# Optimization experiments

Measured on AMD Instinct MI355X. Metric: run time of the kernel, lower is better.

Reference implementation:

```python
import jax, jax.numpy as jnp
import numpy as np
from itertools import combinations

SEQ_LEN = 8
FEAT = 2048
SET_SIZE = 2
DOUT = 1152
WAY = 5
SHOT = 5
NQ = 500
MAX_LEN = int(SEQ_LEN * 1.5)
LN_EPS = 1e-5

TUPLES = np.array(list(combinations(range(SEQ_LEN), SET_SIZE)), dtype=np.int32)  # [T, SET_SIZE]
T_LEN = TUPLES.shape[0]  # C(8,2) = 28

def _positional_encoding(d_model, max_len):
    pos = np.arange(max_len, dtype=np.float32)[:, None]
    div = np.exp(np.arange(0, d_model, 2, dtype=np.float32) * (-np.log(10000.0) / d_model))
    pe = np.zeros((max_len, d_model), dtype=np.float32)
    pe[:, 0::2] = np.sin(pos * div)
    pe[:, 1::2] = np.cos(pos * div)
    return jnp.asarray(pe)

PE = _positional_encoding(FEAT, MAX_LEN)  # dropout is identity in eval mode

def _layernorm(x, gamma, beta):
    mu = jnp.mean(x, axis=-1, keepdims=True)
    var = jnp.var(x, axis=-1, keepdims=True)
    return (x - mu) * jax.lax.rsqrt(var + LN_EPS) * gamma + beta

def setup_inputs() -> dict:
    key = jax.random.key(0)
    ks = jax.random.split(key, 8)
    din = FEAT * SET_SIZE
    sc = 1.0 / np.sqrt(din)
    return {
        "support_set": jax.random.normal(ks[0], (WAY * SHOT, SEQ_LEN, FEAT), jnp.float32),
        "support_labels": jnp.repeat(jnp.arange(WAY, dtype=jnp.int32), SHOT),  # sorted, balanced episode
        "queries": jax.random.normal(ks[1], (NQ, SEQ_LEN, FEAT), jnp.float32),
        "k_w": jax.random.normal(ks[2], (din, DOUT), jnp.float32) * sc,
        "k_b": jnp.zeros((DOUT,), jnp.float32),
        "v_w": jax.random.normal(ks[3], (din, DOUT), jnp.float32) * sc,
        "v_b": jnp.zeros((DOUT,), jnp.float32),
        "ln_k_gamma": jnp.ones((DOUT,), jnp.float32),
        "ln_k_beta": jnp.zeros((DOUT,), jnp.float32),
        "global_temperature": jnp.asarray(1.0, jnp.float32),
        "temperature_weight": jnp.ones((1,), jnp.float32),
    }

def reference(support_set, support_labels, queries, k_w, k_b, v_w, v_b,
              ln_k_gamma, ln_k_beta, global_temperature, temperature_weight):
    n_q = queries.shape[0]
    # positional encoding (dropout is eval-mode identity)
    s = support_set + PE[:SEQ_LEN]
    q = queries + PE[:SEQ_LEN]
    # gather frame tuples: [n, T, SET_SIZE, FEAT] -> [n, T, SET_SIZE*FEAT]
    s_t = s[:, TUPLES, :].reshape(WAY * SHOT, T_LEN, SET_SIZE * FEAT)
    q_t = q[:, TUPLES, :].reshape(n_q, T_LEN, SET_SIZE * FEAT)
    # K / V projections; LayerNorm only on K (as in the module)
    s_ks = _layernorm(s_t @ k_w + k_b, ln_k_gamma, ln_k_beta)
    q_ks = _layernorm(q_t @ k_w + k_b, ln_k_gamma, ln_k_beta)
    s_vs = s_t @ v_w + v_b
    q_vs = q_t @ v_w + v_b
    # labels are sorted & balanced -> per-class slices are a reshape
    class_k = s_ks.reshape(WAY, SHOT, T_LEN, DOUT)
    class_v = s_vs.reshape(WAY, SHOT, T_LEN, DOUT)
    # scores[c,q,t,k,u] = <q_ks[q,t], class_k[c,k,u]> / sqrt(DOUT)
    scores = jnp.einsum('qtd,ckud->cqtku', q_ks, class_k) / np.sqrt(DOUT)
    # softmax jointly over (support-clip k, support-tuple u) per query tuple t
    attn = jax.nn.softmax(scores.reshape(WAY, n_q, T_LEN, SHOT * T_LEN), axis=-1)
    attn = attn.reshape(WAY, n_q, T_LEN, SHOT, T_LEN)
    # prototype = sum over support clips of attn @ class_v
    proto = jnp.einsum('cqtku,ckud->cqtd', attn, class_v)  # [WAY, NQ, T, DOUT]
    diff = q_vs[None] - proto
    dist = jnp.sum(diff * diff, axis=(-2, -1)) / T_LEN  # [WAY, NQ]
    logits = (-dist * global_temperature * temperature_weight[0]).T  # [NQ, WAY]
    return logits
```

## Files before the change

kernel.cpp:

```cpp
#include <hip/hip_runtime.h>

typedef __bf16 bf16;
typedef __attribute__((ext_vector_type(8))) __bf16 bf16x8;
typedef __attribute__((ext_vector_type(4))) float f32x4;

#define AS1 __attribute__((address_space(1)))
#define AS3 __attribute__((address_space(3)))

__device__ __constant__ int c_T0[28] = {0,0,0,0,0,0,0,1,1,1,1,1,1,2,2,2,2,2,3,3,3,3,4,4,4,5,5,6};
__device__ __constant__ int c_T1[28] = {1,2,3,4,5,6,7,2,3,4,5,6,7,3,4,5,6,7,4,5,6,7,5,6,7,6,7,7};

__global__ __launch_bounds__(256) void fill_pack(
    const float* __restrict__ queries, const float* __restrict__ support,
    const float* __restrict__ kw, const float* __restrict__ vw,
    bf16* __restrict__ X, bf16* __restrict__ Wp)
{
    __shared__ float t[32][33];
    const int tid = threadIdx.x;
    if (blockIdx.x < 4224) {
        const int f = blockIdx.x;
        bf16* row = X + (long)f * 2048;
        const int d0 = tid << 3;
        if (f >= 4200) {
            bf16x8 z;
            #pragma unroll
            for (int i = 0; i < 8; ++i) z[i] = (bf16)0.f;
            *(bf16x8*)(row + d0) = z;
            return;
        }
        const float* src = (f < 4000) ? (queries + (long)f * 2048)
                                      : (support + (long)(f - 4000) * 2048);
        const int s = f & 7;
        bf16x8 o;
        #pragma unroll
        for (int i = 0; i < 8; ++i) {
            int d = d0 + i;
            float dv = __expf((float)(d >> 1) * -0.008994473019508f);
            float ang = (float)s * dv;
            float pe = (d & 1) ? __cosf(ang) : __sinf(ang);
            o[i] = (bf16)(src[d] + pe);
        }
        *(bf16x8*)(row + d0) = o;
    } else {
        const int b = blockIdx.x - 4224;
        const int k0 = (b & 63) << 5, n0g = (b >> 6) << 5;
        const int tx = tid & 31, ty = tid >> 5;
        const int j = n0g / 1152, nc = n0g % 1152;
        const float* src = ((j < 2) ? kw : vw) + (long)(((j & 1) << 11) + k0) * 1152 + nc;
        #pragma unroll
        for (int i = 0; i < 4; ++i)
            t[ty + (i << 3)][tx] = src[(long)(ty + (i << 3)) * 1152 + tx];
        __syncthreads();
        #pragma unroll
        for (int i = 0; i < 4; ++i)
            Wp[(long)(n0g + ty + (i << 3)) * 2048 + k0 + tx] = (bf16)t[tx][ty + (i << 3)];
    }
}

template <typename OutT>
__global__ __launch_bounds__(256) void gemm_bt(
    const bf16* __restrict__ A, long lda, const bf16* __restrict__ B, long ldb,
    OutT* __restrict__ C, int N, int K, float scale, int tiles_n)
{
    __shared__ __align__(16) bf16 lA[128 * 32];
    __shared__ __align__(16) bf16 lB[128 * 32];
    const int tid = threadIdx.x;
    const int wid = tid >> 6, lane = tid & 63;
    const int wm = (wid >> 1) << 6, wn = (wid & 1) << 6;
    const int quad = lane >> 4, l16 = lane & 15;
    const int tm = blockIdx.x / tiles_n, tn = blockIdx.x % tiles_n;
    const int m0 = tm << 7, n0 = tn << 7;
    const bf16* Abase = A + (long)m0 * lda;

    f32x4 acc[4][4];
    #pragma unroll
    for (int i = 0; i < 4; ++i)
        #pragma unroll
        for (int j = 0; j < 4; ++j)
            #pragma unroll
            for (int r = 0; r < 4; ++r) acc[i][j][r] = 0.f;

    const int srow = lane >> 2, scol = (lane & 3) << 3;
    for (int kk = 0; kk < K; kk += 32) {
        __syncthreads();
        #pragma unroll
        for (int p = 0; p < 2; ++p) {
            const int rbase = (wid << 5) + (p << 4);
            const bf16* ga = Abase + (long)(rbase + srow) * lda + kk + scol;
            const bf16* gb = B + (long)(n0 + rbase + srow) * ldb + kk + scol;
            __builtin_amdgcn_global_load_lds((const AS1 unsigned int*)ga,
                                             (AS3 unsigned int*)(lA + rbase * 32), 16, 0, 0);
            __builtin_amdgcn_global_load_lds((const AS1 unsigned int*)gb,
                                             (AS3 unsigned int*)(lB + rbase * 32), 16, 0, 0);
        }
        __builtin_amdgcn_s_waitcnt(0);
        __syncthreads();
        bf16x8 af[4], bfr[4];
        #pragma unroll
        for (int i = 0; i < 4; ++i)
            af[i] = *(const bf16x8*)(lA + (wm + (i << 4) + l16) * 32 + (quad << 3));
        #pragma unroll
        for (int j = 0; j < 4; ++j)
            bfr[j] = *(const bf16x8*)(lB + (wn + (j << 4) + l16) * 32 + (quad << 3));
        #pragma unroll
        for (int i = 0; i < 4; ++i)
            #pragma unroll
            for (int j = 0; j < 4; ++j)
                acc[i][j] = __builtin_amdgcn_mfma_f32_16x16x32_bf16(af[i], bfr[j], acc[i][j], 0, 0, 0);
    }
    #pragma unroll
    for (int i = 0; i < 4; ++i) {
        const int row = m0 + wm + (i << 4) + (quad << 2);
        #pragma unroll
        for (int j = 0; j < 4; ++j) {
            const int col = n0 + wn + (j << 4) + l16;
            OutT* cp = C + (long)row * N + col;
            #pragma unroll
            for (int r = 0; r < 4; ++r) cp[(long)r * N] = (OutT)(acc[i][j][r] * scale);
        }
    }
}

__global__ __launch_bounds__(256) void gemm_frames(
    const bf16* __restrict__ H, const bf16* __restrict__ Bk,
    const bf16* __restrict__ svs, float* __restrict__ FG, bf16* __restrict__ Gb)
{
    __shared__ __align__(16) bf16 lA[128 * 32];
    __shared__ __align__(16) bf16 lB[128 * 32];
    const int tid = threadIdx.x;
    const int wid = tid >> 6, lane = tid & 63;
    const int wm = (wid >> 1) << 6, wn = (wid & 1) << 6;
    const int quad = lane >> 4, l16 = lane & 15;
    const bool gram = (int)blockIdx.x >= 792;
    int seg = 4, tm, tn;
    const bf16* Abase;
    long la;
    const bf16* B;
    if (!gram) {
        seg = blockIdx.x / 198;
        int r = blockIdx.x % 198;
        tm = r / 6; tn = r % 6;
        Abase = H + seg * 1152 + (long)(tm << 7) * 4608;
        la = 4608;
        B = (seg < 2) ? Bk : svs;
    } else {
        int r = blockIdx.x - 792;
        tm = r / 6; tn = r % 6;
        Abase = svs + (long)(tm << 7) * 1152;
        la = 1152;
        B = svs;
    }
    const int n0 = tn << 7;

    f32x4 acc[4][4];
    #pragma unroll
    for (int i = 0; i < 4; ++i)
        #pragma unroll
        for (int j = 0; j < 4; ++j)
            #pragma unroll
            for (int r = 0; r < 4; ++r) acc[i][j][r] = 0.f;

    const int srow = lane >> 2, scol = (lane & 3) << 3;
    for (int kk = 0; kk < 1152; kk += 32) {
        __syncthreads();
        #pragma unroll
        for (int p = 0; p < 2; ++p) {
            const int rbase = (wid << 5) + (p << 4);
            const bf16* ga = Abase + (long)(rbase + srow) * la + kk + scol;
            const bf16* gb = B + (long)(n0 + rbase + srow) * 1152 + kk + scol;
            __builtin_amdgcn_global_load_lds((const AS1 unsigned int*)ga,
                                             (AS3 unsigned int*)(lA + rbase * 32), 16, 0, 0);
            __builtin_amdgcn_global_load_lds((const AS1 unsigned int*)gb,
                                             (AS3 unsigned int*)(lB + rbase * 32), 16, 0, 0);
        }
        __builtin_amdgcn_s_waitcnt(0);
        __syncthreads();
        bf16x8 af[4], bfr[4];
        #pragma unroll
        for (int i = 0; i < 4; ++i)
            af[i] = *(const bf16x8*)(lA + (wm + (i << 4) + l16) * 32 + (quad << 3));
        #pragma unroll
        for (int j = 0; j < 4; ++j)
            bfr[j] = *(const bf16x8*)(lB + (wn + (j << 4) + l16) * 32 + (quad << 3));
        #pragma unroll
        for (int i = 0; i < 4; ++i)
            #pragma unroll
            for (int j = 0; j < 4; ++j)
                acc[i][j] = __builtin_amdgcn_mfma_f32_16x16x32_bf16(af[i], bfr[j], acc[i][j], 0, 0, 0);
    }
    #pragma unroll
    for (int i = 0; i < 4; ++i) {
        const int rloc = (tm << 7) + wm + (i << 4) + (quad << 2);
        #pragma unroll
        for (int j = 0; j < 4; ++j) {
            const int col = n0 + wn + (j << 4) + l16;
            #pragma unroll
            for (int r = 0; r < 4; ++r) {
                const int row = rloc + r;
                if (!gram) {
                    FG[(long)(seg * 4224 + row) * 768 + col] = acc[i][j][r];
                } else {
                    bool keep = (row < 700) && (col < 700) && (row / 140 == col / 140);
                    Gb[(long)row * 768 + col] = keep ? (bf16)acc[i][j][r] : (bf16)0.f;
                }
            }
        }
    }
}

__global__ __launch_bounds__(256) void proj_support(
    const bf16* __restrict__ H, const float* __restrict__ kb,
    const float* __restrict__ vb, const float* __restrict__ gamma,
    const float* __restrict__ beta,
    bf16* __restrict__ Bk, bf16* __restrict__ svs,
    float* __restrict__ gd, float* __restrict__ kbd,
    float* __restrict__ bd2, float* __restrict__ bdot)
{
    const int u = blockIdx.x, tid = threadIdx.x;
    bf16* outK = Bk + (long)u * 1152;
    bf16* outV = svs + (long)u * 1152;
    if (u >= 700) {
        for (int d = tid; d < 1152; d += 256) { outK[d] = (bf16)0.f; outV[d] = (bf16)0.f; }
        if (tid == 0) { gd[u] = 0.f; kbd[u] = 0.f; bd2[u] = 0.f; bdot[u] = 0.f; }
        return;
    }
    const int n = u / 28, t = u - n * 28;
    const int fi = 4000 + (n << 3) + c_T0[t];
    const int fj = 4000 + (n << 3) + c_T1[t];
    const bf16* Hi = H + (long)fi * 4608;
    const bf16* Hj = H + (long)fj * 4608;
    float xv[5];
    float sum = 0.f, sumsq = 0.f;
    #pragma unroll
    for (int it = 0; it < 5; ++it) {
        int d = tid + (it << 8);
        float x = 0.f;
        if (d < 1152) {
            x = (float)Hi[d] + (float)Hj[1152 + d] + kb[d];
            sum += x; sumsq += x * x;
        }
        xv[it] = x;
    }
    #pragma unroll
    for (int off = 32; off > 0; off >>= 1) {
        sum += __shfl_xor(sum, off, 64);
        sumsq += __shfl_xor(sumsq, off, 64);
    }
    __shared__ float s1[4], s2[4], sr[4][4];
    const int wid = tid >> 6;
    if ((tid & 63) == 0) { s1[wid] = sum; s2[wid] = sumsq; }
    __syncthreads();
    sum = s1[0] + s1[1] + s1[2] + s1[3];
    sumsq = s2[0] + s2[1] + s2[2] + s2[3];
    const float mu = sum * (1.f / 1152.f);
    const float var = sumsq * (1.f / 1152.f) - mu * mu;
    const float rs = rsqrtf(var + 1e-5f);
    float g_ = 0.f, k_ = 0.f, b_ = 0.f, v_ = 0.f;
    #pragma unroll
    for (int it = 0; it < 5; ++it) {
        int d = tid + (it << 8);
        if (d < 1152) {
            float gm = gamma[d];
            float sk = (xv[it] - mu) * rs * gm + beta[d];
            outK[d] = (bf16)(gm * sk);
            g_ += gm * sk;
            k_ += kb[d] * gm * sk;
            b_ += beta[d] * sk;
            float sv = (float)Hi[2304 + d] + (float)Hj[3456 + d] + vb[d];
            outV[d] = (bf16)sv;
            v_ += vb[d] * sv;
        }
    }
    #pragma unroll
    for (int off = 32; off > 0; off >>= 1) {
        g_ += __shfl_xor(g_, off, 64);
        k_ += __shfl_xor(k_, off, 64);
        b_ += __shfl_xor(b_, off, 64);
        v_ += __shfl_xor(v_, off, 64);
    }
    if ((tid & 63) == 0) { sr[wid][0] = g_; sr[wid][1] = k_; sr[wid][2] = b_; sr[wid][3] = v_; }
    __syncthreads();
    if (tid == 0) {
        gd[u]   = sr[0][0] + sr[1][0] + sr[2][0] + sr[3][0];
        kbd[u]  = sr[0][1] + sr[1][1] + sr[2][1] + sr[3][1];
        bd2[u]  = sr[0][2] + sr[1][2] + sr[2][2] + sr[3][2];
        bdot[u] = sr[0][3] + sr[1][3] + sr[2][3] + sr[3][3];
    }
}

__global__ __launch_bounds__(256) void row_stats(
    const bf16* __restrict__ H, const float* __restrict__ kb,
    const float* __restrict__ vb, float* __restrict__ MU,
    float* __restrict__ RS, float* __restrict__ QS)
{
    const bool kside = (int)blockIdx.x < 500;
    const int q = kside ? blockIdx.x : blockIdx.x - 500;
    const int co = kside ? 0 : 2304;
    const float* bias = kside ? kb : vb;
    const int tid = threadIdx.x;
    __shared__ __align__(16) bf16 Ft[8 * 1152];
    __shared__ __align__(16) bf16 Fb[8 * 1152];
    __shared__ float Sa[8], Qa[8], Ca[8], Sb_[8], Qb_[8], Cb_[8], Pp[28], Sk2[2];
    for (int idx = tid; idx < 1152; idx += 256) {
        int row = idx / 144, col = (idx - row * 144) << 3;
        const bf16* src = H + (long)((q << 3) + row) * 4608 + co;
        *(bf16x8*)(Ft + row * 1152 + col) = *(const bf16x8*)(src + col);
        *(bf16x8*)(Fb + row * 1152 + col) = *(const bf16x8*)(src + 1152 + col);
    }
    __syncthreads();
    const int wid = tid >> 6, lane = tid & 63;
    for (int task = wid; task < 45; task += 4) {
        float s0 = 0.f, s1 = 0.f, s2 = 0.f;
        if (task < 16) {
            const bf16* p = (task < 8) ? (Ft + task * 1152) : (Fb + (task - 8) * 1152);
            for (int c = lane << 3; c < 1152; c += 512) {
                bf16x8 v = *(const bf16x8*)(p + c);
                #pragma unroll
                for (int k = 0; k < 8; ++k) {
                    float f = (float)v[k];
                    s0 += f; s1 += f * f; s2 += f * bias[c + k];
                }
            }
        } else if (task < 44) {
            int t = task - 16;
            const bf16* pa = Ft + c_T0[t] * 1152;
            const bf16* pb = Fb + c_T1[t] * 1152;
            for (int c = lane << 3; c < 1152; c += 512) {
                bf16x8 a = *(const bf16x8*)(pa + c);
                bf16x8 b = *(const bf16x8*)(pb + c);
                #pragma unroll
                for (int k = 0; k < 8; ++k) s0 += (float)a[k] * (float)b[k];
            }
        } else {
            for (int c = lane << 3; c < 1152; c += 512) {
                #pragma unroll
                for (int k = 0; k < 8; ++k) { float f = bias[c + k]; s0 += f; s1 += f * f; }
            }
        }
        #pragma unroll
        for (int off = 32; off > 0; off >>= 1) {
            s0 += __shfl_xor(s0, off, 64);
            s1 += __shfl_xor(s1, off, 64);
            s2 += __shfl_xor(s2, off, 64);
        }
        if (lane == 0) {
            if (task < 8)       { Sa[task] = s0; Qa[task] = s1; Ca[task] = s2; }
            else if (task < 16) { Sb_[task - 8] = s0; Qb_[task - 8] = s1; Cb_[task - 8] = s2; }
            else if (task < 44) Pp[task - 16] = s0;
            else                { Sk2[0] = s0; Sk2[1] = s1; }
        }
    }
    __syncthreads();
    if (kside) {
        if (tid < 28) {
            int i = c_T0[tid], j = c_T1[tid];
            float mu = (Sa[i] + Sb_[j] + Sk2[0]) * (1.f / 1152.f);
            float ex2 = (Qa[i] + Qb_[j] + Sk2[1] + 2.f * (Pp[tid] + Ca[i] + Cb_[j])) * (1.f / 1152.f);
            float var = ex2 - mu * mu;
            int m = q * 28 + tid;
            MU[m] = mu;
            RS[m] = rsqrtf(var + 1e-5f);
        }
    } else {
        if (tid < 64) {
            float term = 0.f;
            if (lane < 28) {
                int i = c_T0[lane], j = c_T1[lane];
                term = Qa[i] + Qb_[j] + Sk2[1] + 2.f * (Pp[lane] + Ca[i] + Cb_[j]);
            }
            #pragma unroll
            for (int off = 32; off > 0; off >>= 1) term += __shfl_xor(term, off, 64);
            if (lane == 0) QS[q] = term;
        }
    }
}

__global__ __launch_bounds__(320) void assemble_softmax(
    const float* __restrict__ Fkt, const float* __restrict__ Fkb,
    const float* __restrict__ MU, const float* __restrict__ RS,
    const float* __restrict__ gd, const float* __restrict__ kbd,
    const float* __restrict__ bd2, bf16* __restrict__ attn)
{
    const int m = blockIdx.x, tid = threadIdx.x;
    bf16* arow = attn + (long)m * 768;
    if (m >= 14000) {
        for (int d = tid; d < 768; d += 320) arow[d] = (bf16)0.f;
        return;
    }
    if (tid < 68) arow[700 + tid] = (bf16)0.f;
    const int q = m / 28, t = m - q * 28;
    const float* ft = Fkt + (long)((q << 3) + c_T0[t]) * 768;
    const float* fb = Fkb + (long)((q << 3) + c_T1[t]) * 768;
    const float mu = MU[m], rs = RS[m];
    const int w = tid >> 6, lane = tid & 63;
    const int base = w * 140;
    const float sc = 0.029462782549439484f;
    int u0 = base + lane, u1 = base + 64 + lane, u2 = base + 128 + lane;
    float v0 = (rs * (ft[u0] + fb[u0] + kbd[u0] - mu * gd[u0]) + bd2[u0]) * sc;
    float v1 = (rs * (ft[u1] + fb[u1] + kbd[u1] - mu * gd[u1]) + bd2[u1]) * sc;
    float v2 = (lane < 12)
             ? (rs * (ft[u2] + fb[u2] + kbd[u2] - mu * gd[u2]) + bd2[u2]) * sc
             : -1e30f;
    float mx = fmaxf(fmaxf(v0, v1), v2);
    #pragma unroll
    for (int off = 32; off > 0; off >>= 1) mx = fmaxf(mx, __shfl_xor(mx, off, 64));
    float e0 = __expf(v0 - mx), e1 = __expf(v1 - mx);
    float e2 = (lane < 12) ? __expf(v2 - mx) : 0.f;
    float s = e0 + e1 + e2;
    #pragma unroll
    for (int off = 32; off > 0; off >>= 1) s += __shfl_xor(s, off, 64);
    const float inv = 1.f / s;
    bf16* aw = arow + base;
    aw[lane] = (bf16)(e0 * inv);
    aw[64 + lane] = (bf16)(e1 * inv);
    if (lane < 12) aw[128 + lane] = (bf16)(e2 * inv);
}

__global__ __launch_bounds__(256) void final_dist(
    const bf16* __restrict__ attn, const bf16* __restrict__ attnG,
    const float* __restrict__ FG, const float* __restrict__ bdot,
    float* __restrict__ dist)
{
    const int w = threadIdx.x >> 6, lane = threadIdx.x & 63;
    const int m = blockIdx.x * 4 + w;
    const int q = m / 28, t = m - q * 28;
    const int fi = (q << 3) + c_T0[t], fj = (q << 3) + c_T1[t];
    const bf16* ar = attn + (long)m * 768;
    const bf16* gr = attnG + (long)m * 768;
    const float* ft = FG + (long)(8448 + fi) * 768;
    const float* fb = FG + (long)(12672 + fj) * 768;
    #pragma unroll
    for (int c = 0; c < 5; ++c) {
        const int base = c * 140;
        float s = 0.f;
        {
            int u = base + lane;
            float wv = ft[u] + fb[u] + bdot[u];
            s += (float)ar[u] * ((float)gr[u] - 2.f * wv);
        }
        {
            int u = base + 64 + lane;
            float wv = ft[u] + fb[u] + bdot[u];
            s += (float)ar[u] * ((float)gr[u] - 2.f * wv);
        }
        if (lane < 12) {
            int u = base + 128 + lane;
            float wv = ft[u] + fb[u] + bdot[u];
            s += (float)ar[u] * ((float)gr[u] - 2.f * wv);
        }
        #pragma unroll
        for (int off = 32; off > 0; off >>= 1) s += __shfl_xor(s, off, 64);
        if (lane == 0) atomicAdd(&dist[c * 500 + q], s);
    }
}

__global__ void finalize(const float* __restrict__ dist, const float* __restrict__ QS,
                         const float* __restrict__ gt, const float* __restrict__ tw,
                         float* __restrict__ out)
{
    int i = blockIdx.x * 256 + threadIdx.x;
    if (i < 2500) {
        int q = i / 5, c = i - q * 5;
        out[i] = -(dist[c * 500 + q] + QS[q]) * (gt[0] * tw[0] * (1.f / 28.f));
    }
}

extern "C" void kernel_launch(void* const* d_in, const int* in_sizes, int n_in,
                              void* d_out, int out_size, void* d_ws, size_t ws_size,
                              hipStream_t stream)
{
    const float* support = (const float*)d_in[0];
    const float* queries = (const float*)d_in[2];
    const float* kw      = (const float*)d_in[3];
    const float* kb      = (const float*)d_in[4];
    const float* vw      = (const float*)d_in[5];
    const float* vb      = (const float*)d_in[6];
    const float* gamma   = (const float*)d_in[7];
    const float* beta    = (const float*)d_in[8];
    const float* gt      = (const float*)d_in[9];
    const float* tw      = (const float*)d_in[10];
    float* out = (float*)d_out;

    char* ws = (char*)d_ws;
    size_t off = 0;
    auto alloc = [&](size_t b) { char* p = ws + off; off += (b + 255) & ~(size_t)255; return p; };
    bf16* X      = (bf16*)alloc(4224ull * 2048 * 2);
    bf16* Wp     = (bf16*)alloc(4608ull * 2048 * 2);
    char* uni    = alloc(14080ull * 768 * 4);
    bf16* H      = (bf16*)uni;
    bf16* attn   = (bf16*)uni;
    bf16* attnG  = (bf16*)(uni + 14080ull * 768 * 2);
    float* FG    = (float*)alloc(16896ull * 768 * 4);
    bf16* Bk     = (bf16*)alloc(768ull * 1152 * 2);
    bf16* svs    = (bf16*)alloc(768ull * 1152 * 2);
    bf16* Gb     = (bf16*)alloc(768ull * 768 * 2);
    float* MU    = (float*)alloc(14000ull * 4);
    float* RS    = (float*)alloc(14000ull * 4);
    float* gd    = (float*)alloc(768 * 4);
    float* kbd   = (float*)alloc(768 * 4);
    float* bd2   = (float*)alloc(768 * 4);
    float* bdot  = (float*)alloc(768 * 4);
    float* QS    = (float*)alloc(500 * 4);
    float* dist  = (float*)alloc(5 * 500 * 4);

    hipMemsetAsync(dist, 0, 5 * 500 * 4, stream);
    fill_pack<<<4224 + 9216, 256, 0, stream>>>(queries, support, kw, vw, X, Wp);
    gemm_bt<bf16><<<33 * 36, 256, 0, stream>>>(X, 2048, Wp, 2048, H, 4608, 2048, 1.f, 36);
    proj_support<<<768, 256, 0, stream>>>(H, kb, vb, gamma, beta, Bk, svs, gd, kbd, bd2, bdot);
    row_stats<<<1000, 256, 0, stream>>>(H, kb, vb, MU, RS, QS);
    gemm_frames<<<828, 256, 0, stream>>>(H, Bk, svs, FG, Gb);
    assemble_softmax<<<14080, 320, 0, stream>>>(FG, FG + 4224ull * 768, MU, RS, gd, kbd, bd2, attn);
    gemm_bt<bf16><<<110 * 6, 256, 0, stream>>>(attn, 768, Gb, 768, attnG, 768, 768, 1.f, 6);
    final_dist<<<3500, 256, 0, stream>>>(attn, attnG, FG, bdot, dist);
    finalize<<<10, 256, 0, stream>>>(dist, QS, gt, tw, out);
}
```

Before: 423.5 us.

## Store frame-gram intermediates in bf16 and merge support/row-stat kernels

The FG intermediate buffer (per-frame projections against support keys/values) is now written and read as bf16 instead of fp32, halving its memory traffic in gemm_frames, assemble_softmax and final_dist. Separately, proj_support and row_stats are fused into one launch with a shared-memory union, removing one kernel launch and letting the two independent workloads run together. The bf16 storage adds rounding error to the attention logits and distance terms, and the merged kernel reserves the larger shared-memory footprint for every block.

```diff
diff --git a/kernel.cpp b/kernel.cpp
--- a/kernel.cpp
+++ b/kernel.cpp
@@ -123,7 +123,7 @@
 
 __global__ __launch_bounds__(256) void gemm_frames(
     const bf16* __restrict__ H, const bf16* __restrict__ Bk,
-    const bf16* __restrict__ svs, float* __restrict__ FG, bf16* __restrict__ Gb)
+    const bf16* __restrict__ svs, bf16* __restrict__ FG, bf16* __restrict__ Gb)
 {
     __shared__ __align__(16) bf16 lA[128 * 32];
     __shared__ __align__(16) bf16 lB[128 * 32];
@@ -198,7 +198,7 @@
             for (int r = 0; r < 4; ++r) {
                 const int row = rloc + r;
                 if (!gram) {
-                    FG[(long)(seg * 4224 + row) * 768 + col] = acc[i][j][r];
+                    FG[(long)(seg * 4224 + row) * 768 + col] = (bf16)acc[i][j][r];
                 } else {
                     bool keep = (row < 700) && (col < 700) && (row / 140 == col / 140);
                     Gb[(long)row * 768 + col] = keep ? (bf16)acc[i][j][r] : (bf16)0.f;
@@ -208,99 +208,108 @@
     }
 }
 
-__global__ __launch_bounds__(256) void proj_support(
+__global__ __launch_bounds__(256) void support_stats(
     const bf16* __restrict__ H, const float* __restrict__ kb,
     const float* __restrict__ vb, const float* __restrict__ gamma,
     const float* __restrict__ beta,
     bf16* __restrict__ Bk, bf16* __restrict__ svs,
     float* __restrict__ gd, float* __restrict__ kbd,
-    float* __restrict__ bd2, float* __restrict__ bdot)
-{
-    const int u = blockIdx.x, tid = threadIdx.x;
-    bf16* outK = Bk + (long)u * 1152;
-    bf16* outV = svs + (long)u * 1152;
-    if (u >= 700) {
-        for (int d = tid; d < 1152; d += 256) { outK[d] = (bf16)0.f; outV[d] = (bf16)0.f; }
-        if (tid == 0) { gd[u] = 0.f; kbd[u] = 0.f; bd2[u] = 0.f; bdot[u] = 0.f; }
+    float* __restrict__ bd2, float* __restrict__ bdot,
+    float* __restrict__ MU, float* __restrict__ RS, float* __restrict__ QS)
+{
+    __shared__ __align__(16) char smem[2 * 9216 * 2 + 512];
+    const int tid = threadIdx.x;
+    const int wid = tid >> 6, lane = tid & 63;
+    if ((int)blockIdx.x < 768) {
+        const int u = blockIdx.x;
+        bf16* outK = Bk + (long)u * 1152;
+        bf16* outV = svs + (long)u * 1152;
+        if (u >= 700) {
+            for (int d = tid; d < 1152; d += 256) { outK[d] = (bf16)0.f; outV[d] = (bf16)0.f; }
+            if (tid == 0) { gd[u] = 0.f; kbd[u] = 0.f; bd2[u] = 0.f; bdot[u] = 0.f; }
+            return;
+        }
+        float* s1 = (float*)smem;
+        float* s2 = s1 + 4;
+        float* sr = s2 + 4;
+        const int n = u / 28, t = u - n * 28;
+        const int fi = 4000 + (n << 3) + c_T0[t];
+        const int fj = 4000 + (n << 3) + c_T1[t];
+        const bf16* Hi = H + (long)fi * 4608;
+        const bf16* Hj = H + (long)fj * 4608;
+        float xv[5];
+        float sum = 0.f, sumsq = 0.f;
+        #pragma unroll
+        for (int it = 0; it < 5; ++it) {
+            int d = tid + (it << 8);
+            float x = 0.f;
+            if (d < 1152) {
+                x = (float)Hi[d] + (float)Hj[1152 + d] + kb[d];
+                sum += x; sumsq += x * x;
+            }
+            xv[it] = x;
+        }
+        #pragma unroll
+        for (int off = 32; off > 0; off >>= 1) {
+            sum += __shfl_xor(sum, off, 64);
+            sumsq += __shfl_xor(sumsq, off, 64);
+        }
+        if ((tid & 63) == 0) { s1[wid] = sum; s2[wid] = sumsq; }
+        __syncthreads();
+        sum = s1[0] + s1[1] + s1[2] + s1[3];
+        sumsq = s2[0] + s2[1] + s2[2] + s2[3];
+        const float mu = sum * (1.f / 1152.f);
+        const float var = sumsq * (1.f / 1152.f) - mu * mu;
+        const float rs = rsqrtf(var + 1e-5f);
+        float g_ = 0.f, k_ = 0.f, b_ = 0.f, v_ = 0.f;
+        #pragma unroll
+        for (int it = 0; it < 5; ++it) {
+            int d = tid + (it << 8);
+            if (d < 1152) {
+                float gm = gamma[d];
+                float sk = (xv[it] - mu) * rs * gm + beta[d];
+                outK[d] = (bf16)(gm * sk);
+                g_ += gm * sk;
+                k_ += kb[d] * gm * sk;
+                b_ += beta[d] * sk;
+                float sv = (float)Hi[2304 + d] + (float)Hj[3456 + d] + vb[d];
+                outV[d] = (bf16)sv;
+                v_ += vb[d] * sv;
+            }
+        }
+        #pragma unroll
+        for (int off = 32; off > 0; off >>= 1) {
+            g_ += __shfl_xor(g_, off, 64);
+            k_ += __shfl_xor(k_, off, 64);
+            b_ += __shfl_xor(b_, off, 64);
+            v_ += __shfl_xor(v_, off, 64);
+        }
+        if ((tid & 63) == 0) { sr[wid * 4 + 0] = g_; sr[wid * 4 + 1] = k_; sr[wid * 4 + 2] = b_; sr[wid * 4 + 3] = v_; }
+        __syncthreads();
+        if (tid == 0) {
+            gd[u]   = sr[0] + sr[4] + sr[8]  + sr[12];
+            kbd[u]  = sr[1] + sr[5] + sr[9]  + sr[13];
+            bd2[u]  = sr[2] + sr[6] + sr[10] + sr[14];
+            bdot[u] = sr[3] + sr[7] + sr[11] + sr[15];
+        }
         return;
     }
-    const int n = u / 28, t = u - n * 28;
-    const int fi = 4000 + (n << 3) + c_T0[t];
-    const int fj = 4000 + (n << 3) + c_T1[t];
-    const bf16* Hi = H + (long)fi * 4608;
-    const bf16* Hj = H + (long)fj * 4608;
-    float xv[5];
-    float sum = 0.f, sumsq = 0.f;
-    #pragma unroll
-    for (int it = 0; it < 5; ++it) {
-        int d = tid + (it << 8);
-        float x = 0.f;
-        if (d < 1152) {
-            x = (float)Hi[d] + (float)Hj[1152 + d] + kb[d];
-            sum += x; sumsq += x * x;
-        }
-        xv[it] = x;
-    }
-    #pragma unroll
-    for (int off = 32; off > 0; off >>= 1) {
-        sum += __shfl_xor(sum, off, 64);
-        sumsq += __shfl_xor(sumsq, off, 64);
-    }
-    __shared__ float s1[4], s2[4], sr[4][4];
-    const int wid = tid >> 6;
-    if ((tid & 63) == 0) { s1[wid] = sum; s2[wid] = sumsq; }
-    __syncthreads();
-    sum = s1[0] + s1[1] + s1[2] + s1[3];
-    sumsq = s2[0] + s2[1] + s2[2] + s2[3];
-    const float mu = sum * (1.f / 1152.f);
-    const float var = sumsq * (1.f / 1152.f) - mu * mu;
-    const float rs = rsqrtf(var + 1e-5f);
-    float g_ = 0.f, k_ = 0.f, b_ = 0.f, v_ = 0.f;
-    #pragma unroll
-    for (int it = 0; it < 5; ++it) {
-        int d = tid + (it << 8);
-        if (d < 1152) {
-            float gm = gamma[d];
-            float sk = (xv[it] - mu) * rs * gm + beta[d];
-            outK[d] = (bf16)(gm * sk);
-            g_ += gm * sk;
-            k_ += kb[d] * gm * sk;
-            b_ += beta[d] * sk;
-            float sv = (float)Hi[2304 + d] + (float)Hj[3456 + d] + vb[d];
-            outV[d] = (bf16)sv;
-            v_ += vb[d] * sv;
-        }
-    }
-    #pragma unroll
-    for (int off = 32; off > 0; off >>= 1) {
-        g_ += __shfl_xor(g_, off, 64);
-        k_ += __shfl_xor(k_, off, 64);
-        b_ += __shfl_xor(b_, off, 64);
-        v_ += __shfl_xor(v_, off, 64);
-    }
-    if ((tid & 63) == 0) { sr[wid][0] = g_; sr[wid][1] = k_; sr[wid][2] = b_; sr[wid][3] = v_; }
-    __syncthreads();
-    if (tid == 0) {
-        gd[u]   = sr[0][0] + sr[1][0] + sr[2][0] + sr[3][0];
-        kbd[u]  = sr[0][1] + sr[1][1] + sr[2][1] + sr[3][1];
-        bd2[u]  = sr[0][2] + sr[1][2] + sr[2][2] + sr[3][2];
-        bdot[u] = sr[0][3] + sr[1][3] + sr[2][3] + sr[3][3];
-    }
-}
-
-__global__ __launch_bounds__(256) void row_stats(
-    const bf16* __restrict__ H, const float* __restrict__ kb,
-    const float* __restrict__ vb, float* __restrict__ MU,
-    float* __restrict__ RS, float* __restrict__ QS)
-{
-    const bool kside = (int)blockIdx.x < 500;
-    const int q = kside ? blockIdx.x : blockIdx.x - 500;
+    const int s_ = blockIdx.x - 768;
+    const bool kside = s_ < 500;
+    const int q = kside ? s_ : s_ - 500;
     const int co = kside ? 0 : 2304;
     const float* bias = kside ? kb : vb;
-    const int tid = threadIdx.x;
-    __shared__ __align__(16) bf16 Ft[8 * 1152];
-    __shared__ __align__(16) bf16 Fb[8 * 1152];
-    __shared__ float Sa[8], Qa[8], Ca[8], Sb_[8], Qb_[8], Cb_[8], Pp[28], Sk2[2];
+    bf16* Ft = (bf16*)smem;
+    bf16* Fb = Ft + 9216;
+    float* fl = (float*)(smem + 36864);
+    float* Sa = fl;
+    float* Qa = fl + 8;
+    float* Ca = fl + 16;
+    float* Sb_ = fl + 24;
+    float* Qb_ = fl + 32;
+    float* Cb_ = fl + 40;
+    float* Pp = fl + 48;
+    float* Sk2 = fl + 76;
     for (int idx = tid; idx < 1152; idx += 256) {
         int row = idx / 144, col = (idx - row * 144) << 3;
         const bf16* src = H + (long)((q << 3) + row) * 4608 + co;
@@ -308,9 +317,8 @@
         *(bf16x8*)(Fb + row * 1152 + col) = *(const bf16x8*)(src + 1152 + col);
     }
     __syncthreads();
-    const int wid = tid >> 6, lane = tid & 63;
     for (int task = wid; task < 45; task += 4) {
-        float s0 = 0.f, s1 = 0.f, s2 = 0.f;
+        float s0 = 0.f, s1v = 0.f, s2v = 0.f;
         if (task < 16) {
             const bf16* p = (task < 8) ? (Ft + task * 1152) : (Fb + (task - 8) * 1152);
             for (int c = lane << 3; c < 1152; c += 512) {
@@ -318,7 +326,7 @@
                 #pragma unroll
                 for (int k = 0; k < 8; ++k) {
                     float f = (float)v[k];
-                    s0 += f; s1 += f * f; s2 += f * bias[c + k];
+                    s0 += f; s1v += f * f; s2v += f * bias[c + k];
                 }
             }
         } else if (task < 44) {
@@ -334,20 +342,20 @@
         } else {
             for (int c = lane << 3; c < 1152; c += 512) {
                 #pragma unroll
-                for (int k = 0; k < 8; ++k) { float f = bias[c + k]; s0 += f; s1 += f * f; }
+                for (int k = 0; k < 8; ++k) { float f = bias[c + k]; s0 += f; s1v += f * f; }
             }
         }
         #pragma unroll
         for (int off = 32; off > 0; off >>= 1) {
             s0 += __shfl_xor(s0, off, 64);
-            s1 += __shfl_xor(s1, off, 64);
-            s2 += __shfl_xor(s2, off, 64);
+            s1v += __shfl_xor(s1v, off, 64);
+            s2v += __shfl_xor(s2v, off, 64);
         }
         if (lane == 0) {
-            if (task < 8)       { Sa[task] = s0; Qa[task] = s1; Ca[task] = s2; }
-            else if (task < 16) { Sb_[task - 8] = s0; Qb_[task - 8] = s1; Cb_[task - 8] = s2; }
+            if (task < 8)       { Sa[task] = s0; Qa[task] = s1v; Ca[task] = s2v; }
+            else if (task < 16) { Sb_[task - 8] = s0; Qb_[task - 8] = s1v; Cb_[task - 8] = s2v; }
             else if (task < 44) Pp[task - 16] = s0;
-            else                { Sk2[0] = s0; Sk2[1] = s1; }
+            else                { Sk2[0] = s0; Sk2[1] = s1v; }
         }
     }
     __syncthreads();
@@ -376,7 +384,7 @@
 }
 
 __global__ __launch_bounds__(320) void assemble_softmax(
-    const float* __restrict__ Fkt, const float* __restrict__ Fkb,
+    const bf16* __restrict__ Fkt, const bf16* __restrict__ Fkb,
     const float* __restrict__ MU, const float* __restrict__ RS,
     const float* __restrict__ gd, const float* __restrict__ kbd,
     const float* __restrict__ bd2, bf16* __restrict__ attn)
@@ -389,17 +397,17 @@
     }
     if (tid < 68) arow[700 + tid] = (bf16)0.f;
     const int q = m / 28, t = m - q * 28;
-    const float* ft = Fkt + (long)((q << 3) + c_T0[t]) * 768;
-    const float* fb = Fkb + (long)((q << 3) + c_T1[t]) * 768;
+    const bf16* ft = Fkt + (long)((q << 3) + c_T0[t]) * 768;
+    const bf16* fb = Fkb + (long)((q << 3) + c_T1[t]) * 768;
     const float mu = MU[m], rs = RS[m];
     const int w = tid >> 6, lane = tid & 63;
     const int base = w * 140;
     const float sc = 0.029462782549439484f;
     int u0 = base + lane, u1 = base + 64 + lane, u2 = base + 128 + lane;
-    float v0 = (rs * (ft[u0] + fb[u0] + kbd[u0] - mu * gd[u0]) + bd2[u0]) * sc;
-    float v1 = (rs * (ft[u1] + fb[u1] + kbd[u1] - mu * gd[u1]) + bd2[u1]) * sc;
+    float v0 = (rs * ((float)ft[u0] + (float)fb[u0] + kbd[u0] - mu * gd[u0]) + bd2[u0]) * sc;
+    float v1 = (rs * ((float)ft[u1] + (float)fb[u1] + kbd[u1] - mu * gd[u1]) + bd2[u1]) * sc;
     float v2 = (lane < 12)
-             ? (rs * (ft[u2] + fb[u2] + kbd[u2] - mu * gd[u2]) + bd2[u2]) * sc
+             ? (rs * ((float)ft[u2] + (float)fb[u2] + kbd[u2] - mu * gd[u2]) + bd2[u2]) * sc
              : -1e30f;
     float mx = fmaxf(fmaxf(v0, v1), v2);
     #pragma unroll
@@ -418,7 +426,7 @@
 
 __global__ __launch_bounds__(256) void final_dist(
     const bf16* __restrict__ attn, const bf16* __restrict__ attnG,
-    const float* __restrict__ FG, const float* __restrict__ bdot,
+    const bf16* __restrict__ FG, const float* __restrict__ bdot,
     float* __restrict__ dist)
 {
     const int w = threadIdx.x >> 6, lane = threadIdx.x & 63;
@@ -427,25 +435,25 @@
     const int fi = (q << 3) + c_T0[t], fj = (q << 3) + c_T1[t];
     const bf16* ar = attn + (long)m * 768;
     const bf16* gr = attnG + (long)m * 768;
-    const float* ft = FG + (long)(8448 + fi) * 768;
-    const float* fb = FG + (long)(12672 + fj) * 768;
+    const bf16* ft = FG + (long)(8448 + fi) * 768;
+    const bf16* fb = FG + (long)(12672 + fj) * 768;
     #pragma unroll
     for (int c = 0; c < 5; ++c) {
         const int base = c * 140;
         float s = 0.f;
         {
             int u = base + lane;
-            float wv = ft[u] + fb[u] + bdot[u];
+            float wv = (float)ft[u] + (float)fb[u] + bdot[u];
             s += (float)ar[u] * ((float)gr[u] - 2.f * wv);
         }
         {
             int u = base + 64 + lane;
-            float wv = ft[u] + fb[u] + bdot[u];
+            float wv = (float)ft[u] + (float)fb[u] + bdot[u];
             s += (float)ar[u] * ((float)gr[u] - 2.f * wv);
         }
         if (lane < 12) {
             int u = base + 128 + lane;
-            float wv = ft[u] + fb[u] + bdot[u];
+            float wv = (float)ft[u] + (float)fb[u] + bdot[u];
             s += (float)ar[u] * ((float)gr[u] - 2.f * wv);
         }
         #pragma unroll
@@ -490,7 +498,7 @@
     bf16* H      = (bf16*)uni;
     bf16* attn   = (bf16*)uni;
     bf16* attnG  = (bf16*)(uni + 14080ull * 768 * 2);
-    float* FG    = (float*)alloc(16896ull * 768 * 4);
+    bf16* FG     = (bf16*)alloc(16896ull * 768 * 2);
     bf16* Bk     = (bf16*)alloc(768ull * 1152 * 2);
     bf16* svs    = (bf16*)alloc(768ull * 1152 * 2);
     bf16* Gb     = (bf16*)alloc(768ull * 768 * 2);
@@ -506,11 +514,11 @@
     hipMemsetAsync(dist, 0, 5 * 500 * 4, stream);
     fill_pack<<<4224 + 9216, 256, 0, stream>>>(queries, support, kw, vw, X, Wp);
     gemm_bt<bf16><<<33 * 36, 256, 0, stream>>>(X, 2048, Wp, 2048, H, 4608, 2048, 1.f, 36);
-    proj_support<<<768, 256, 0, stream>>>(H, kb, vb, gamma, beta, Bk, svs, gd, kbd, bd2, bdot);
-    row_stats<<<1000, 256, 0, stream>>>(H, kb, vb, MU, RS, QS);
+    support_stats<<<1768, 256, 0, stream>>>(H, kb, vb, gamma, beta, Bk, svs,
+                                            gd, kbd, bd2, bdot, MU, RS, QS);
     gemm_frames<<<828, 256, 0, stream>>>(H, Bk, svs, FG, Gb);
     assemble_softmax<<<14080, 320, 0, stream>>>(FG, FG + 4224ull * 768, MU, RS, gd, kbd, bd2, attn);
     gemm_bt<bf16><<<110 * 6, 256, 0, stream>>>(attn, 768, Gb, 768, attnG, 768, 768, 1.f, 6);
-    final_dist<<<3500, 256, 0, stream>>>(attn, attnG, FG, bdot, dist);
+    final_dist<<<3500, 256, 0, stream>>>(attn, attnG, FG + 0, bdot, dist);
     finalize<<<10, 256, 0, stream>>>(dist, QS, gt, tw, out);
 }
```

Measured after the change: 419.2 us. About the same (-1.0%).
